# Performance work log

Hardware: AMD Instinct MI355X
Metric: run time of the kernel (lower is better)

## Reference

```python
import jax, jax.numpy as jnp
from jax import lax
import numpy as np

POOL = 4
STRIDE = 2


def _window_sum(x, k, s):
    # x: [B,H,W,1] -> sliding-window sum over kxk spatial windows, VALID padding
    return lax.reduce_window(x, jnp.float32(0.0), lax.add,
                             window_dimensions=(1, k, k, 1),
                             window_strides=(1, s, s, 1),
                             padding='VALID')


def setup_inputs() -> dict:
    key = jax.random.key(0)
    x = jax.random.normal(key, (64, 1024, 1024, 1), dtype=jnp.float32)
    return {"input_data": x}


def reference(input_data) -> jnp.ndarray:
    # Equivalent to: extract_patches(kxk, stride s, VALID) -> reduce_std over each window.
    # Computed without materializing patches: std = sqrt(E[x^2] - E[x]^2) per window.
    k, s = POOL, STRIDE
    n = jnp.float32(k * k)
    wsum = _window_sum(input_data, k, s)            # [B,Ho,Wo,1]
    wsumsq = _window_sum(input_data * input_data, k, s)
    mean = wsum / n
    var = jnp.maximum(wsumsq / n - mean * mean, 0.0)
    std = jnp.sqrt(var)                              # [B,Ho,Wo,1]
    b, ho, wo, _ = std.shape
    return std.reshape(b, ho * wo)                   # matches (B, H_out*W_out)
```

## Files before the change

kernel.cpp:

```cpp
#include <hip/hip_runtime.h>


#define IN_H 1024
#define IN_W 1024
#define OUT_H 511
#define OUT_W 511

__global__ __launch_bounds__(256) void stdpool_kernel(
    const float* __restrict__ in, float* __restrict__ out) {
  const int tx = threadIdx.x;
  const int ty = threadIdx.y;
  const int tileX = blockIdx.x * 16 + tx;
  const int tileY = blockIdx.y * 16 + ty;
  const int b = blockIdx.z;

  const int wo0 = tileX * 4;
  const int ho0 = tileY * 4;
  const int col0 = wo0 * 2;
  const int row0 = ho0 * 2;

  const float* __restrict__ src = in + (size_t)b * IN_H * IN_W;

  float s[4][4];
  float ss[4][4];
#pragma unroll
  for (int j = 0; j < 4; ++j)
#pragma unroll
    for (int c = 0; c < 4; ++c) {
      s[j][c] = 0.0f;
      ss[j][c] = 0.0f;
    }

  const bool have_tail = (col0 + 9) < IN_W;

#pragma unroll
  for (int r = 0; r < 10; ++r) {
    const int rg = row0 + r;
    if (rg < IN_H) {
      const float* __restrict__ rp = src + (size_t)rg * IN_W + col0;
      const float4 a = *(const float4*)(rp);
      const float4 d = *(const float4*)(rp + 4);
      float c8 = 0.0f, c9 = 0.0f;
      if (have_tail) {
        const float2 t = *(const float2*)(rp + 8);
        c8 = t.x;
        c9 = t.y;
      }
      const float cv[10] = {a.x, a.y, a.z, a.w, d.x, d.y, d.z, d.w, c8, c9};

      float p[5], q[5];
#pragma unroll
      for (int i = 0; i < 5; ++i) {
        p[i] = cv[2 * i] + cv[2 * i + 1];
        q[i] = cv[2 * i] * cv[2 * i] + cv[2 * i + 1] * cv[2 * i + 1];
      }
      float hw[4], hq[4];
#pragma unroll
      for (int c = 0; c < 4; ++c) {
        hw[c] = p[c] + p[c + 1];
        hq[c] = q[c] + q[c + 1];
      }

#pragma unroll
      for (int j = 0; j < 4; ++j) {
        if (r >= 2 * j && r <= 2 * j + 3) {
#pragma unroll
          for (int c = 0; c < 4; ++c) {
            s[j][c] += hw[c];
            ss[j][c] += hq[c];
          }
        }
      }
    }
  }

  const float inv_n = 1.0f / 16.0f;
  float* __restrict__ obase = out + (size_t)b * OUT_H * OUT_W;
#pragma unroll
  for (int j = 0; j < 4; ++j) {
    const int ho = ho0 + j;
    if (ho < OUT_H) {
      float* __restrict__ orow = obase + (size_t)ho * OUT_W + wo0;
#pragma unroll
      for (int c = 0; c < 4; ++c) {
        const int wo = wo0 + c;
        if (wo < OUT_W) {
          const float mean = s[j][c] * inv_n;
          float var = ss[j][c] * inv_n - mean * mean;
          var = fmaxf(var, 0.0f);
          orow[c] = sqrtf(var);
        }
      }
    }
  }
}

extern "C" void kernel_launch(void* const* d_in, const int* in_sizes, int n_in,
                              void* d_out, int out_size, void* d_ws,
                              size_t ws_size, hipStream_t stream) {
  const float* x = (const float*)d_in[0];
  float* out = (float*)d_out;

  dim3 block(16, 16, 1);
  dim3 grid(8, 8, 64);
  stdpool_kernel<<<grid, block, 0, stream>>>(x, out);
}
```

Measured before the change: 388.9 us.

## Restructure std-pool as row-strip sweep with rolling sums and wavefront shuffles

Replaces the per-thread 4x4 output tile with one block per 16-output-row strip per image. Each thread covers 4 input columns and walks down the rows, reusing the previous row-pair's partial sums. Horizontal window overlap is filled by a cross-lane shuffle, with a tail load at wavefront boundaries. This removes the redundant reads of overlapping input rows and columns and gives coalesced row-wise access. The trade-off is a serial loop with a software-prefetched next row and a narrower grid.

Result: no change. 393.8 us (+1.3%).

```diff
diff --git a/kernel.cpp b/kernel.cpp
--- a/kernel.cpp
+++ b/kernel.cpp
@@ -5,93 +5,76 @@
 #define IN_W 1024
 #define OUT_H 511
 #define OUT_W 511
+#define STRIPS 32
+#define ROWS_PER_STRIP 16
 
-__global__ __launch_bounds__(256) void stdpool_kernel(
+__global__ __launch_bounds__(256, 8) void stdpool_kernel(
     const float* __restrict__ in, float* __restrict__ out) {
-  const int tx = threadIdx.x;
-  const int ty = threadIdx.y;
-  const int tileX = blockIdx.x * 16 + tx;
-  const int tileY = blockIdx.y * 16 + ty;
-  const int b = blockIdx.z;
+  const int tid = threadIdx.x;
+  const int w = tid >> 6;
+  const int l = tid & 63;
+  const int strip = blockIdx.x;
+  const int b = blockIdx.y;
 
-  const int wo0 = tileX * 4;
-  const int ho0 = tileY * 4;
-  const int col0 = wo0 * 2;
-  const int row0 = ho0 * 2;
+  const int col0 = w * 256 + l * 4;
+  const int o0 = w * 128 + l * 2;
+  const bool has_o1 = (o0 + 1) < OUT_W;
+  const bool tail = (l == 63) && has_o1;
+
+  const int j0 = strip * ROWS_PER_STRIP;
+  const int jn = min(ROWS_PER_STRIP, OUT_H - j0);
+  const int t0 = j0, t1 = j0 + jn;
 
   const float* __restrict__ src = in + (size_t)b * IN_H * IN_W;
+  float* __restrict__ dst = out + (size_t)b * OUT_H * OUT_W;
 
-  float s[4][4];
-  float ss[4][4];
-#pragma unroll
-  for (int j = 0; j < 4; ++j)
-#pragma unroll
-    for (int c = 0; c < 4; ++c) {
-      s[j][c] = 0.0f;
-      ss[j][c] = 0.0f;
+  const float* rp = src + (size_t)(2 * t0) * IN_W + col0;
+  float4 a = *(const float4*)rp;
+  float4 c = *(const float4*)(rp + IN_W);
+
+  float Pp0 = 0.f, Pp1 = 0.f, Qp0 = 0.f, Qp1 = 0.f;
+
+  for (int t = t0; t <= t1; ++t) {
+    float4 na = make_float4(0.f, 0.f, 0.f, 0.f);
+    float4 nc = na;
+    if (t < t1) {
+      const float* np = src + (size_t)(2 * (t + 1)) * IN_W + col0;
+      na = *(const float4*)np;
+      nc = *(const float4*)(np + IN_W);
     }
 
-  const bool have_tail = (col0 + 9) < IN_W;
+    float c0 = (a.x + a.y) + (c.x + c.y);
+    float c1 = (a.z + a.w) + (c.z + c.w);
+    float d0 = fmaf(a.y, a.y, a.x * a.x) + fmaf(c.y, c.y, c.x * c.x);
+    float d1 = fmaf(a.w, a.w, a.z * a.z) + fmaf(c.w, c.w, c.z * c.z);
 
-#pragma unroll
-  for (int r = 0; r < 10; ++r) {
-    const int rg = row0 + r;
-    if (rg < IN_H) {
-      const float* __restrict__ rp = src + (size_t)rg * IN_W + col0;
-      const float4 a = *(const float4*)(rp);
-      const float4 d = *(const float4*)(rp + 4);
-      float c8 = 0.0f, c9 = 0.0f;
-      if (have_tail) {
-        const float2 t = *(const float2*)(rp + 8);
-        c8 = t.x;
-        c9 = t.y;
-      }
-      const float cv[10] = {a.x, a.y, a.z, a.w, d.x, d.y, d.z, d.w, c8, c9};
+    float cn = __shfl_down(c0, 1, 64);
+    float dn = __shfl_down(d0, 1, 64);
+    if (tail) {
+      const float* tp = src + (size_t)(2 * t) * IN_W + col0 + 4;
+      const float2 e0 = *(const float2*)tp;
+      const float2 e1 = *(const float2*)(tp + IN_W);
+      cn = (e0.x + e0.y) + (e1.x + e1.y);
+      dn = fmaf(e0.y, e0.y, e0.x * e0.x) + fmaf(e1.y, e1.y, e1.x * e1.x);
+    }
 
-      float p[5], q[5];
-#pragma unroll
-      for (int i = 0; i < 5; ++i) {
-        p[i] = cv[2 * i] + cv[2 * i + 1];
-        q[i] = cv[2 * i] * cv[2 * i] + cv[2 * i + 1] * cv[2 * i + 1];
-      }
-      float hw[4], hq[4];
-#pragma unroll
-      for (int c = 0; c < 4; ++c) {
-        hw[c] = p[c] + p[c + 1];
-        hq[c] = q[c] + q[c + 1];
-      }
+    const float P0 = c0 + c1, P1 = c1 + cn;
+    const float Q0 = d0 + d1, Q1 = d1 + dn;
 
-#pragma unroll
-      for (int j = 0; j < 4; ++j) {
-        if (r >= 2 * j && r <= 2 * j + 3) {
-#pragma unroll
-          for (int c = 0; c < 4; ++c) {
-            s[j][c] += hw[c];
-            ss[j][c] += hq[c];
-          }
-        }
-      }
+    if (t > t0) {
+      const float inv = 1.0f / 16.0f;
+      const float s0 = Pp0 + P0, s1 = Pp1 + P1;
+      const float q0 = Qp0 + Q0, q1 = Qp1 + Q1;
+      const float m0 = s0 * inv, m1 = s1 * inv;
+      const float v0 = fmaxf(fmaf(-m0, m0, q0 * inv), 0.0f);
+      const float v1 = fmaxf(fmaf(-m1, m1, q1 * inv), 0.0f);
+      float* op = dst + (size_t)(t - 1) * OUT_W + o0;
+      op[0] = sqrtf(v0);
+      if (has_o1) op[1] = sqrtf(v1);
     }
-  }
 
-  const float inv_n = 1.0f / 16.0f;
-  float* __restrict__ obase = out + (size_t)b * OUT_H * OUT_W;
-#pragma unroll
-  for (int j = 0; j < 4; ++j) {
-    const int ho = ho0 + j;
-    if (ho < OUT_H) {
-      float* __restrict__ orow = obase + (size_t)ho * OUT_W + wo0;
-#pragma unroll
-      for (int c = 0; c < 4; ++c) {
-        const int wo = wo0 + c;
-        if (wo < OUT_W) {
-          const float mean = s[j][c] * inv_n;
-          float var = ss[j][c] * inv_n - mean * mean;
-          var = fmaxf(var, 0.0f);
-          orow[c] = sqrtf(var);
-        }
-      }
-    }
+    Pp0 = P0; Pp1 = P1; Qp0 = Q0; Qp1 = Q1;
+    a = na; c = nc;
   }
 }
 
@@ -101,7 +84,7 @@
   const float* x = (const float*)d_in[0];
   float* out = (float*)d_out;
 
-  dim3 block(16, 16, 1);
-  dim3 grid(8, 8, 64);
+  dim3 block(256, 1, 1);
+  dim3 grid(STRIPS, 64, 1);
   stdpool_kernel<<<grid, block, 0, stream>>>(x, out);
 }
```
